# Optimization experiments

Measured on AMD Instinct MI355X. Metric: run time of the kernel, lower is better.

The kernel has to match this reference:

```python
import jax, jax.numpy as jnp
import numpy as np

POOL = 7          # cf.pool_size
SR = 2            # roi_align sampling_ratio
LEVELS = [0, 1, 2, 3]
C = 192           # cf.end_filts
HC = 2            # cf.head_classes
RF = 1
N_ROIS = 1000
B = 4


def roi_align_2d(fmap, boxes, batch_inds, pool_size=POOL, sr=SR):
    """Bilinear RoIAlign. fmap [B,C,H,W]; boxes [N,4] = (y1,x1,y2,x2) in fmap pixel coords."""
    _, _, H, W = fmap.shape
    y1, x1, y2, x2 = boxes[:, 0], boxes[:, 1], boxes[:, 2], boxes[:, 3]
    bin_h = jnp.maximum(y2 - y1, 1.0) / pool_size
    bin_w = jnp.maximum(x2 - x1, 1.0) / pool_size
    # sampling offsets within the roi, [pool*sr]
    grid = (jnp.arange(pool_size, dtype=jnp.float32)[:, None]
            + (jnp.arange(sr, dtype=jnp.float32)[None, :] + 0.5) / sr).reshape(-1)
    ys = y1[:, None] + grid[None, :] * bin_h[:, None]   # [N, P*S]
    xs = x1[:, None] + grid[None, :] * bin_w[:, None]   # [N, P*S]
    y = jnp.broadcast_to(ys[:, :, None], (ys.shape[0], ys.shape[1], xs.shape[1]))  # [N,PS,PS]
    x = jnp.broadcast_to(xs[:, None, :], y.shape)
    valid = (y >= -1.0) & (y <= H) & (x >= -1.0) & (x <= W)
    y = jnp.clip(y, 0.0, H - 1)
    x = jnp.clip(x, 0.0, W - 1)
    y0 = jnp.floor(y).astype(jnp.int32)
    x0 = jnp.floor(x).astype(jnp.int32)
    y1i = jnp.minimum(y0 + 1, H - 1)
    x1i = jnp.minimum(x0 + 1, W - 1)
    ly = y - y0
    lx = x - x0
    b = batch_inds[:, None, None]
    f00 = fmap[b, :, y0, x0]    # [N,PS,PS,C]
    f01 = fmap[b, :, y0, x1i]
    f10 = fmap[b, :, y1i, x0]
    f11 = fmap[b, :, y1i, x1i]
    w00 = ((1 - ly) * (1 - lx))[..., None]
    w01 = ((1 - ly) * lx)[..., None]
    w10 = (ly * (1 - lx))[..., None]
    w11 = (ly * lx)[..., None]
    val = (f00 * w00 + f01 * w01 + f10 * w10 + f11 * w11) * valid[..., None]
    n = val.shape[0]
    val = val.reshape(n, pool_size, sr, pool_size, sr, -1).mean(axis=(2, 4))  # [N,P,P,C]
    return jnp.transpose(val, (0, 3, 1, 2))  # [N,C,P,P]


def pyramid_roi_align(fmaps, rois, pool_size=POOL, levels=LEVELS):
    boxes = jax.lax.stop_gradient(rois[:, :4])  # level_boxes.detach() in original
    batch_ix = rois[:, 4].astype(jnp.int32)
    h = boxes[:, 2] - boxes[:, 0]
    w = boxes[:, 3] - boxes[:, 1]
    roi_level = jnp.clip(jnp.round(4.0 + jnp.log2(jnp.sqrt(h * w))),
                         levels[0], levels[-1]).astype(jnp.int32)
    pooled = jnp.zeros((boxes.shape[0], fmaps[0].shape[1], pool_size, pool_size), fmaps[0].dtype)
    for li, lvl in enumerate(levels):
        H, W = fmaps[li].shape[2], fmaps[li].shape[3]
        scale = jnp.asarray([H, W, H, W], jnp.float32)
        p = roi_align_2d(fmaps[li], boxes * scale, batch_ix, pool_size)
        pooled = jnp.where((roi_level == lvl)[:, None, None, None], p, pooled)
    return pooled


def setup_inputs() -> dict:
    key = jax.random.key(0)
    ks = jax.random.split(key, 20)
    fmap0 = jax.random.normal(ks[0], (B, C, 128, 128), jnp.float32)
    fmap1 = jax.random.normal(ks[1], (B, C, 64, 64), jnp.float32)
    fmap2 = jax.random.normal(ks[2], (B, C, 32, 32), jnp.float32)
    fmap3 = jax.random.normal(ks[3], (B, C, 16, 16), jnp.float32)
    # valid normalized rois: (y1,x1,y2,x2,batch_ix)
    cy = jax.random.uniform(ks[4], (N_ROIS,), minval=0.15, maxval=0.85)
    cx = jax.random.uniform(ks[5], (N_ROIS,), minval=0.15, maxval=0.85)
    hh = jax.random.uniform(ks[6], (N_ROIS,), minval=0.02, maxval=0.15)
    hw = jax.random.uniform(ks[7], (N_ROIS,), minval=0.02, maxval=0.15)
    bix = jax.random.randint(ks[8], (N_ROIS,), 0, B).astype(jnp.float32)
    rois = jnp.stack([jnp.clip(cy - hh, 0, 1), jnp.clip(cx - hw, 0, 1),
                      jnp.clip(cy + hh, 0, 1), jnp.clip(cx + hw, 0, 1), bix], axis=1)
    d = C * 4  # 768
    s1 = 1.0 / np.sqrt(C * POOL * POOL)
    s2 = 1.0 / np.sqrt(d)
    params = dict(
        w1=jax.random.normal(ks[9], (d, C, POOL, POOL), jnp.float32) * s1,
        b1=jnp.zeros((d,), jnp.float32),
        w2=jax.random.normal(ks[10], (d, d), jnp.float32) * s2,
        b2=jnp.zeros((d,), jnp.float32),
        w_bbox=jax.random.normal(ks[11], (HC * 4, d), jnp.float32) * s2,
        b_bbox=jnp.zeros((HC * 4,), jnp.float32),
        w_cls=jax.random.normal(ks[12], (HC, d), jnp.float32) * s2,
        b_cls=jnp.zeros((HC,), jnp.float32),
        w_reg=jax.random.normal(ks[13], (HC * RF, d), jnp.float32) * s2,
        b_reg=jnp.zeros((HC * RF,), jnp.float32),
        w_unc=jax.random.normal(ks[14], (HC, d), jnp.float32) * s2,
        b_unc=jnp.zeros((HC,), jnp.float32),
    )
    return dict(fmap0=fmap0, fmap1=fmap1, fmap2=fmap2, fmap3=fmap3, rois=rois, **params)


def reference(fmap0, fmap1, fmap2, fmap3, rois, w1, b1, w2, b2,
              w_bbox, b_bbox, w_cls, b_cls, w_reg, b_reg, w_unc, b_unc):
    x = pyramid_roi_align([fmap0, fmap1, fmap2, fmap3], rois)      # [N,C,7,7]
    x = jax.nn.relu(jnp.einsum('ncij,ocij->no', x, w1) + b1)       # conv1 ks=7 -> 1x1
    x = jax.nn.relu(x @ w2.T + b2)                                 # conv2 1x1
    n = x.shape[0]
    mrcnn_bbox = (x @ w_bbox.T + b_bbox).reshape(n, -1, 4)         # [N,HC,2*dim]
    mrcnn_class_logits = x @ w_cls.T + b_cls                       # [N,HC]
    reg = (x @ w_reg.T + b_reg).reshape(n, -1, RF)
    unc = x @ w_unc.T + b_unc
    mrcnn_regress = jnp.concatenate([reg, unc[..., None]], axis=2)  # [N,HC,RF+1]
    return mrcnn_bbox, mrcnn_class_logits, mrcnn_regress
```

## Files before the change

### kernel.cpp

```cpp
#include <hip/hip_runtime.h>
#include <hip/hip_bf16.h>
#include <cstddef>
#include <cstdint>

typedef __attribute__((ext_vector_type(8))) short short8;
typedef __attribute__((ext_vector_type(16))) float float16;

#define C_CH 192
#define PK   9408
#define D1   768

__device__ __forceinline__ ushort f2bf(float v) {
    return __builtin_bit_cast(unsigned short, __float2bfloat16(v));
}

__global__ __launch_bounds__(256) void cvt_bf16_2(
    const float* __restrict__ in1, ushort* __restrict__ out1, int n4_1,
    const float* __restrict__ in2, ushort* __restrict__ out2, int n4_2)
{
    int i = blockIdx.x * 256 + threadIdx.x;
    const float* in; ushort* out;
    if (i < n4_1) { in = in1; out = out1; }
    else          { i -= n4_1; if (i >= n4_2) return; in = in2; out = out2; }
    float4 v = ((const float4*)in)[i];
    ushort4 o;
    o.x = f2bf(v.x); o.y = f2bf(v.y); o.z = f2bf(v.z); o.w = f2bf(v.w);
    ((ushort4*)out)[i] = o;
}

__global__ __launch_bounds__(256) void cvt_bf16(const float* __restrict__ in,
                                                ushort* __restrict__ out, int n4)
{
    int i = blockIdx.x * 256 + threadIdx.x;
    if (i >= n4) return;
    float4 v = ((const float4*)in)[i];
    ushort4 o;
    o.x = f2bf(v.x); o.y = f2bf(v.y); o.z = f2bf(v.z); o.w = f2bf(v.w);
    ((ushort4*)out)[i] = o;
}

__global__ __launch_bounds__(256) void fused_pre(
    const float* __restrict__ f0, const float* __restrict__ f1,
    const float* __restrict__ f2, const float* __restrict__ f3,
    ushort* __restrict__ o0, ushort* __restrict__ o1,
    ushort* __restrict__ o2, ushort* __restrict__ o3,
    const float* __restrict__ w1src, ushort* __restrict__ w1dst, int n41,
    const float* __restrict__ w2src, ushort* __restrict__ w2dst, int n42,
    int nTrans)
{
    __shared__ unsigned int sm[96][33];

    int bx = blockIdx.x;
    if (bx >= nTrans) {
        int i = (bx - nTrans) * 256 + threadIdx.x;
        const float* in; ushort* out;
        if (i < n41) { in = w1src; out = w1dst; }
        else         { i -= n41; if (i >= n42) return; in = w2src; out = w2dst; }
        float4 v = ((const float4*)in)[i];
        ushort4 o;
        o.x = f2bf(v.x); o.y = f2bf(v.y); o.z = f2bf(v.z); o.w = f2bf(v.w);
        ((ushort4*)out)[i] = o;
        return;
    }

    int b = bx / 680;
    int t = bx - b * 680;
    const float* in; ushort* out; int HW, hw0;
    if      (t < 512) { in = f0; out = o0; HW = 16384; hw0 = t * 32; }
    else if (t < 640) { in = f1; out = o1; HW = 4096;  hw0 = (t - 512) * 32; }
    else if (t < 672) { in = f2; out = o2; HW = 1024;  hw0 = (t - 640) * 32; }
    else              { in = f3; out = o3; HW = 256;   hw0 = (t - 672) * 32; }

    int tx = threadIdx.x & 31;
    int ty = threadIdx.x >> 5;

    const float* ip = in + (size_t)b * C_CH * HW + hw0;
    #pragma unroll
    for (int it = 0; it < 12; ++it) {
        int cp = it * 8 + ty;
        float v0 = ip[(size_t)(2 * cp)     * HW + tx];
        float v1 = ip[(size_t)(2 * cp + 1) * HW + tx];
        sm[cp][tx] = (unsigned int)f2bf(v0) | ((unsigned int)f2bf(v1) << 16);
    }
    __syncthreads();

    unsigned int* op = (unsigned int*)(out + ((size_t)b * HW + hw0) * C_CH);
    #pragma unroll
    for (int it = 0; it < 12; ++it) {
        int idx = it * 256 + (int)threadIdx.x;
        int r = idx / 96;
        int p = idx - r * 96;
        op[idx] = sm[p][r];
    }
}

__global__ __launch_bounds__(192) void roi_gather(
    const ushort* __restrict__ n0p, const ushort* __restrict__ n1p,
    const ushort* __restrict__ n2p, const ushort* __restrict__ n3p,
    const float* __restrict__ rois, ushort* __restrict__ pooled)
{
    __shared__ float4 s_patch4[256 * 12];
    __shared__ int    s_off[196][4];
    __shared__ float  s_w[196][4];
    __shared__ ushort s_out[96 * 49];

    const int n    = blockIdx.x >> 1;
    const int half = blockIdx.x & 1;
    const int tid  = threadIdx.x;

    float by1 = rois[n*5+0], bx1 = rois[n*5+1];
    float by2 = rois[n*5+2], bx2 = rois[n*5+3];
    int   b   = (int)rois[n*5+4];

    float hh = by2 - by1, ww = bx2 - bx1;
    int lvl = (int)rintf(4.0f + log2f(sqrtf(hh * ww)));
    lvl = min(max(lvl, 0), 3);

    const ushort* fm; int H;
    if      (lvl == 0) { fm = n0p; H = 128; }
    else if (lvl == 1) { fm = n1p; H = 64;  }
    else if (lvl == 2) { fm = n2p; H = 32;  }
    else               { fm = n3p; H = 16;  }
    float Hf = (float)H;

    float y1p = by1 * Hf, x1p = bx1 * Hf;
    float y2p = by2 * Hf, x2p = bx2 * Hf;
    float bin_h = fmaxf(y2p - y1p, 1.0f) * (1.0f / 7.0f);
    float bin_w = fmaxf(x2p - x1p, 1.0f) * (1.0f / 7.0f);

    float yF = fminf(fmaxf(y1p + 0.25f * bin_h, 0.0f), Hf - 1.0f);
    float yL = fminf(fmaxf(y1p + 6.75f * bin_h, 0.0f), Hf - 1.0f);
    float xF = fminf(fmaxf(x1p + 0.25f * bin_w, 0.0f), Hf - 1.0f);
    float xL = fminf(fmaxf(x1p + 6.75f * bin_w, 0.0f), Hf - 1.0f);
    int ymin = (int)floorf(yF);
    int ymax = min((int)floorf(yL) + 1, H - 1);
    int xmin = (int)floorf(xF);
    int xmax = min((int)floorf(xL) + 1, H - 1);
    int nrows = ymax - ymin + 1;
    int ncols = xmax - xmin + 1;
    int np = nrows * ncols;
    bool usePatch = (np <= 256);

    uintptr_t bp = (uintptr_t)(fm + (size_t)b * H * H * C_CH);
    unsigned int blo = __builtin_amdgcn_readfirstlane((unsigned int)bp);
    unsigned int bhi = __builtin_amdgcn_readfirstlane((unsigned int)(bp >> 32));
    const char* sbase = (const char*)((((uintptr_t)bhi) << 32) | blo);

    for (int s = tid; s < 196; s += 192) {
        int sx = s & 1, sy = (s >> 1) & 1, ij = s >> 2;
        int i = ij / 7, j = ij - i * 7;

        float gy = (float)i + 0.25f + 0.5f * (float)sy;
        float y  = y1p + gy * bin_h;
        bool  vy = (y >= -1.0f) && (y <= Hf);
        float yc = fminf(fmaxf(y, 0.0f), Hf - 1.0f);
        int   y0 = (int)floorf(yc);
        float ly = yc - (float)y0;
        int   y1i = min(y0 + 1, H - 1);

        float gx = (float)j + 0.25f + 0.5f * (float)sx;
        float x  = x1p + gx * bin_w;
        bool  vx = (x >= -1.0f) && (x <= Hf);
        float xc = fminf(fmaxf(x, 0.0f), Hf - 1.0f);
        int   x0 = (int)floorf(xc);
        float lx = xc - (float)x0;
        int   x1i = min(x0 + 1, H - 1);

        float vm = (vy && vx) ? 0.25f : 0.0f;
        if (usePatch) {
            int ry0 = y0 - ymin, ry1 = y1i - ymin;
            int rx0 = x0 - xmin, rx1 = x1i - xmin;
            s_off[s][0] = (ry0 * ncols + rx0) * 48;
            s_off[s][1] = (ry0 * ncols + rx1) * 48;
            s_off[s][2] = (ry1 * ncols + rx0) * 48;
            s_off[s][3] = (ry1 * ncols + rx1) * 48;
        } else {
            s_off[s][0] = (y0  * H + x0 ) * (C_CH * 2);
            s_off[s][1] = (y0  * H + x1i) * (C_CH * 2);
            s_off[s][2] = (y1i * H + x0 ) * (C_CH * 2);
            s_off[s][3] = (y1i * H + x1i) * (C_CH * 2);
        }
        s_w[s][0] = (1.0f - ly) * (1.0f - lx) * vm;
        s_w[s][1] = (1.0f - ly) * lx * vm;
        s_w[s][2] = ly * (1.0f - lx) * vm;
        s_w[s][3] = ly * lx * vm;
    }

    if (usePatch) {
        int pq = tid / 12;
        int pd = tid - pq * 12;
        for (int p0 = 0; p0 < np; p0 += 16) {
            int p = p0 + pq;
            if (p < np) {
                int py = p / ncols;
                int px = p - py * ncols;
                const char* src = sbase +
                    ((size_t)((ymin + py) * H + (xmin + px)) * (C_CH * 2)
                     + half * 192 + pd * 16);
                s_patch4[p * 12 + pd] = *(const float4*)src;
            }
        }
    }
    __syncthreads();

    const int grp = tid / 48;
    const int ci  = tid - grp * 48;
    const int cl  = ci * 2;
    const int bin_lo = grp * 13;
    const int bin_hi = min(bin_lo + 13, 49);

    if (usePatch) {
        const unsigned int* patch_dw = (const unsigned int*)s_patch4;
        for (int bin = bin_lo; bin < bin_hi; ++bin) {
            float a0 = 0.0f, a1 = 0.0f;
            #pragma unroll
            for (int sub = 0; sub < 4; ++sub) {
                int s = bin * 4 + sub;
                #pragma unroll
                for (int tp = 0; tp < 4; ++tp) {
                    unsigned int u = patch_dw[s_off[s][tp] + ci];
                    float w = s_w[s][tp];
                    float lo = __builtin_bit_cast(float, u << 16);
                    float hi = __builtin_bit_cast(float, u & 0xffff0000u);
                    a0 = fmaf(lo, w, a0);
                    a1 = fmaf(hi, w, a1);
                }
            }
            s_out[(cl + 0) * 49 + bin] = f2bf(a0);
            s_out[(cl + 1) * 49 + bin] = f2bf(a1);
        }
    } else {
        const int c4g = half * 192 + ci * 4;
        for (int bin = bin_lo; bin < bin_hi; ++bin) {
            float a0 = 0.0f, a1 = 0.0f;
            #pragma unroll
            for (int sub = 0; sub < 4; ++sub) {
                int s = bin * 4 + sub;
                #pragma unroll
                for (int tp = 0; tp < 4; ++tp) {
                    unsigned int u = *(const unsigned int*)(sbase + (s_off[s][tp] + c4g));
                    float w = s_w[s][tp];
                    float lo = __builtin_bit_cast(float, u << 16);
                    float hi = __builtin_bit_cast(float, u & 0xffff0000u);
                    a0 = fmaf(lo, w, a0);
                    a1 = fmaf(hi, w, a1);
                }
            }
            s_out[(cl + 0) * 49 + bin] = f2bf(a0);
            s_out[(cl + 1) * 49 + bin] = f2bf(a1);
        }
    }
    __syncthreads();

    unsigned int* po = (unsigned int*)(pooled + (size_t)n * PK + half * 4704);
    const unsigned int* so = (const unsigned int*)s_out;
    for (int idx = tid; idx < 2352; idx += 192) po[idx] = so[idx];
}

__global__ __launch_bounds__(256) void roi_align_nchw(
    const float* __restrict__ f0, const float* __restrict__ f1,
    const float* __restrict__ f2, const float* __restrict__ f3,
    const float* __restrict__ rois, ushort* __restrict__ pooled, int n_rois)
{
    int idx = blockIdx.x * 256 + threadIdx.x;
    if (idx >= n_rois * PK) return;
    int n  = idx / PK;
    int r  = idx - n * PK;
    int c  = r / 49;
    int ij = r - c * 49;
    int i  = ij / 7;
    int j  = ij - i * 7;

    float by1 = rois[n*5+0], bx1 = rois[n*5+1];
    float by2 = rois[n*5+2], bx2 = rois[n*5+3];
    int   b   = (int)rois[n*5+4];

    float hh = by2 - by1, ww = bx2 - bx1;
    int lvl = (int)rintf(4.0f + log2f(sqrtf(hh * ww)));
    lvl = min(max(lvl, 0), 3);

    const float* fmap; int H;
    if      (lvl == 0) { fmap = f0; H = 128; }
    else if (lvl == 1) { fmap = f1; H = 64;  }
    else if (lvl == 2) { fmap = f2; H = 32;  }
    else               { fmap = f3; H = 16;  }
    float Hf = (float)H;

    float y1p = by1 * Hf, x1p = bx1 * Hf;
    float bin_h = fmaxf(by2 * Hf - y1p, 1.0f) * (1.0f / 7.0f);
    float bin_w = fmaxf(bx2 * Hf - x1p, 1.0f) * (1.0f / 7.0f);

    const float* base = fmap + ((size_t)b * C_CH + c) * (size_t)(H * H);

    float acc = 0.0f;
    #pragma unroll
    for (int sy = 0; sy < 2; ++sy) {
        float y  = y1p + ((float)i + 0.25f + 0.5f * (float)sy) * bin_h;
        bool  vy = (y >= -1.0f) && (y <= Hf);
        float yc = fminf(fmaxf(y, 0.0f), Hf - 1.0f);
        int   y0 = (int)floorf(yc);
        float ly = yc - (float)y0;
        int   y1i = min(y0 + 1, H - 1);
        #pragma unroll
        for (int sx = 0; sx < 2; ++sx) {
            float x  = x1p + ((float)j + 0.25f + 0.5f * (float)sx) * bin_w;
            bool  vx = (x >= -1.0f) && (x <= Hf);
            float xc = fminf(fmaxf(x, 0.0f), Hf - 1.0f);
            int   x0 = (int)floorf(xc);
            float lx = xc - (float)x0;
            int   x1i = min(x0 + 1, H - 1);
            if (vy && vx) {
                float v = base[y0 * H + x0 ] * (1.0f - ly) * (1.0f - lx)
                        + base[y0 * H + x1i] * (1.0f - ly) * lx
                        + base[y1i * H + x0 ] * ly * (1.0f - lx)
                        + base[y1i * H + x1i] * ly * lx;
                acc += v;
            }
        }
    }
    pooled[idx] = f2bf(acc * 0.25f);
}

template<int MODE>
__global__ __launch_bounds__(256) void mfma_gemm(
    const ushort* __restrict__ A, const ushort* __restrict__ W,
    const float* __restrict__ bias, void* __restrict__ outp,
    int M, int N, int K, int nkPer, int nkTotal)
{
    __shared__ char ldsA[2][8192];
    __shared__ char ldsB[2][8192];

    const int t    = threadIdx.x;
    const int lane = t & 63;
    const int wave = t >> 6;
    const int wm = wave >> 1, wn = wave & 1;

    const int m0 = blockIdx.y * 64;
    const int n0 = blockIdx.x * 64;
    const int kb = (MODE == 2) ? blockIdx.z * nkPer : 0;
    const int nk = (MODE == 2) ? min(nkPer, nkTotal - kb) : nkPer;

    const int ks   = t & 3;
    const int mrow = t >> 2;
    const int g    = mrow >> 5;
    const int rw   = mrow & 31;
    const int lof0 = ks*2048 + g*1024 + ((     rw) ^ (ks<<2))*16;
    const int lof1 = ks*2048 + g*1024 + ((32 + rw) ^ (ks<<2))*16;

    const int arow = min(m0 + mrow, M-1);
    const int brow = n0 + mrow;
    const ushort* ap = A + (size_t)arow * K + (size_t)kb * 64 + ks*16;
    const ushort* bp = W + (size_t)brow * K + (size_t)kb * 64 + ks*16;

    float4 ra0, ra1, rb0, rb1;
    float4 qa0, qa1, qb0, qb1;

    ra0 = ((const float4*)ap)[0]; ra1 = ((const float4*)ap)[1];
    rb0 = ((const float4*)bp)[0]; rb1 = ((const float4*)bp)[1];
    *(float4*)&ldsA[0][lof0] = ra0; *(float4*)&ldsA[0][lof1] = ra1;
    *(float4*)&ldsB[0][lof0] = rb0; *(float4*)&ldsB[0][lof1] = rb1;
    {
        int k1 = min(1, nk - 1);
        const ushort* ap1 = ap + (size_t)k1 * 64;
        const ushort* bp1 = bp + (size_t)k1 * 64;
        ra0 = ((const float4*)ap1)[0]; ra1 = ((const float4*)ap1)[1];
        rb0 = ((const float4*)bp1)[0]; rb1 = ((const float4*)bp1)[1];
    }
    __syncthreads();

    float16 acc = {};

    for (int kt = 0; kt < nk; ++kt) {
        {
            int k2 = min(kt + 2, nk - 1);
            const ushort* ap2 = ap + (size_t)k2 * 64;
            const ushort* bp2 = bp + (size_t)k2 * 64;
            qa0 = ((const float4*)ap2)[0]; qa1 = ((const float4*)ap2)[1];
            qb0 = ((const float4*)bp2)[0]; qb1 = ((const float4*)bp2)[1];
        }
        if (kt + 1 < nk) {
            char* dA = ldsA[(kt+1)&1]; char* dB = ldsB[(kt+1)&1];
            *(float4*)&dA[lof0] = ra0; *(float4*)&dA[lof1] = ra1;
            *(float4*)&dB[lof0] = rb0; *(float4*)&dB[lof1] = rb1;
        }
        const char* sA = ldsA[kt&1]; const char* sB = ldsB[kt&1];
        #pragma unroll
        for (int s = 0; s < 4; ++s) {
            int ro = s*2048 + (lane ^ (s<<2))*16;
            short8 af = *(const short8*)&sA[wm*1024 + ro];
            short8 bf = *(const short8*)&sB[wn*1024 + ro];
            acc = __builtin_amdgcn_mfma_f32_32x32x16_bf16(af, bf, acc, 0, 0, 0);
        }
        __syncthreads();
        ra0 = qa0; ra1 = qa1; rb0 = qb0; rb1 = qb1;
    }

    const int col   = lane & 31;
    const int rbase = 4 * (lane >> 5);
    const int nG    = n0 + wn*32 + col;

    if (MODE == 2) {
        float* O = (float*)outp + (size_t)blockIdx.z * M * N;
        #pragma unroll
        for (int r = 0; r < 16; ++r) {
            int row = (r & 3) + 8*(r >> 2) + rbase;
            int mG  = m0 + wm*32 + row;
            if (mG < M) O[(size_t)mG * N + nG] = acc[r];
        }
    } else if (MODE == 1) {
        const float bv = bias[nG];
        ushort* O = (ushort*)outp;
        #pragma unroll
        for (int r = 0; r < 16; ++r) {
            int row = (r & 3) + 8*(r >> 2) + rbase;
            int mG  = m0 + wm*32 + row;
            if (mG < M) O[(size_t)mG * N + nG] = f2bf(fmaxf(acc[r] + bv, 0.0f));
        }
    } else {
        const float bv = bias[nG];
        float* O = (float*)outp;
        #pragma unroll
        for (int r = 0; r < 16; ++r) {
            int row = (r & 3) + 8*(r >> 2) + rbase;
            int mG  = m0 + wm*32 + row;
            if (mG < M) O[(size_t)mG * N + nG] = fmaxf(acc[r] + bv, 0.0f);
        }
    }
}

__global__ __launch_bounds__(256) void mfma_gemm128(
    const ushort* __restrict__ A, const ushort* __restrict__ W,
    void* __restrict__ outp, int M, int N, int K, int nkPer, int nkTotal)
{
    __shared__ char ldsA[2][16384];
    __shared__ char ldsB[2][16384];

    const int t    = threadIdx.x;
    const int lane = t & 63;
    const int wave = t >> 6;
    const int wm = wave >> 1, wn = wave & 1;

    const int m0 = blockIdx.y * 128;
    const int n0 = blockIdx.x * 128;
    const int kb = blockIdx.z * nkPer;
    const int nk = min(nkPer, nkTotal - kb);

    const int ks   = t & 3;
    const int mrow = t >> 2;
    const int g    = mrow >> 5;
    const int rw   = mrow & 31;
    const int swz  = ks << 2;
    const int lof0 = ks*4096 + g*1024 + ((     rw) ^ swz)*16;
    const int lof1 = ks*4096 + g*1024 + ((32 + rw) ^ swz)*16;

    const int arow0 = min(m0 + mrow,      M-1);
    const int arow1 = min(m0 + mrow + 64, M-1);
    const int brow0 = n0 + mrow;
    const int brow1 = n0 + mrow + 64;
    const ushort* ap0 = A + (size_t)arow0 * K + (size_t)kb * 64 + ks*16;
    const ushort* ap1 = A + (size_t)arow1 * K + (size_t)kb * 64 + ks*16;
    const ushort* bp0 = W + (size_t)brow0 * K + (size_t)kb * 64 + ks*16;
    const ushort* bp1 = W + (size_t)brow1 * K + (size_t)kb * 64 + ks*16;

    float4 ra0, ra1, ra2, ra3, rb0, rb1, rb2, rb3;
    float4 qa0, qa1, qa2, qa3, qb0, qb1, qb2, qb3;

    ra0 = ((const float4*)ap0)[0]; ra1 = ((const float4*)ap0)[1];
    ra2 = ((const float4*)ap1)[0]; ra3 = ((const float4*)ap1)[1];
    rb0 = ((const float4*)bp0)[0]; rb1 = ((const float4*)bp0)[1];
    rb2 = ((const float4*)bp1)[0]; rb3 = ((const float4*)bp1)[1];
    *(float4*)&ldsA[0][lof0]      = ra0; *(float4*)&ldsA[0][lof1]      = ra1;
    *(float4*)&ldsA[0][lof0+2048] = ra2; *(float4*)&ldsA[0][lof1+2048] = ra3;
    *(float4*)&ldsB[0][lof0]      = rb0; *(float4*)&ldsB[0][lof1]      = rb1;
    *(float4*)&ldsB[0][lof0+2048] = rb2; *(float4*)&ldsB[0][lof1+2048] = rb3;
    {
        int k1 = min(1, nk - 1);
        const ushort* a0 = ap0 + (size_t)k1 * 64; const ushort* a1 = ap1 + (size_t)k1 * 64;
        const ushort* b0 = bp0 + (size_t)k1 * 64; const ushort* b1 = bp1 + (size_t)k1 * 64;
        ra0 = ((const float4*)a0)[0]; ra1 = ((const float4*)a0)[1];
        ra2 = ((const float4*)a1)[0]; ra3 = ((const float4*)a1)[1];
        rb0 = ((const float4*)b0)[0]; rb1 = ((const float4*)b0)[1];
        rb2 = ((const float4*)b1)[0]; rb3 = ((const float4*)b1)[1];
    }
    __syncthreads();

    float16 acc00 = {}, acc01 = {}, acc10 = {}, acc11 = {};

    for (int kt = 0; kt < nk; ++kt) {
        {
            int k2 = min(kt + 2, nk - 1);
            const ushort* a0 = ap0 + (size_t)k2 * 64; const ushort* a1 = ap1 + (size_t)k2 * 64;
            const ushort* b0 = bp0 + (size_t)k2 * 64; const ushort* b1 = bp1 + (size_t)k2 * 64;
            qa0 = ((const float4*)a0)[0]; qa1 = ((const float4*)a0)[1];
            qa2 = ((const float4*)a1)[0]; qa3 = ((const float4*)a1)[1];
            qb0 = ((const float4*)b0)[0]; qb1 = ((const float4*)b0)[1];
            qb2 = ((const float4*)b1)[0]; qb3 = ((const float4*)b1)[1];
        }
        if (kt + 1 < nk) {
            char* dA = ldsA[(kt+1)&1]; char* dB = ldsB[(kt+1)&1];
            *(float4*)&dA[lof0]      = ra0; *(float4*)&dA[lof1]      = ra1;
            *(float4*)&dA[lof0+2048] = ra2; *(float4*)&dA[lof1+2048] = ra3;
            *(float4*)&dB[lof0]      = rb0; *(float4*)&dB[lof1]      = rb1;
            *(float4*)&dB[lof0+2048] = rb2; *(float4*)&dB[lof1+2048] = rb3;
        }
        const char* sA = ldsA[kt&1]; const char* sB = ldsB[kt&1];
        #pragma unroll
        for (int s = 0; s < 4; ++s) {
            int ro = s*4096 + (lane ^ (s<<2))*16;
            short8 a0 = *(const short8*)&sA[wm*2048        + ro];
            short8 a1 = *(const short8*)&sA[wm*2048 + 1024 + ro];
            short8 b0 = *(const short8*)&sB[wn*2048        + ro];
            short8 b1 = *(const short8*)&sB[wn*2048 + 1024 + ro];
            acc00 = __builtin_amdgcn_mfma_f32_32x32x16_bf16(a0, b0, acc00, 0, 0, 0);
            acc01 = __builtin_amdgcn_mfma_f32_32x32x16_bf16(a0, b1, acc01, 0, 0, 0);
            acc10 = __builtin_amdgcn_mfma_f32_32x32x16_bf16(a1, b0, acc10, 0, 0, 0);
            acc11 = __builtin_amdgcn_mfma_f32_32x32x16_bf16(a1, b1, acc11, 0, 0, 0);
        }
        __syncthreads();
        ra0 = qa0; ra1 = qa1; ra2 = qa2; ra3 = qa3;
        rb0 = qb0; rb1 = qb1; rb2 = qb2; rb3 = qb3;
    }

    const int col   = lane & 31;
    const int rbase = 4 * (lane >> 5);
    float* O = (float*)outp + (size_t)blockIdx.z * M * N;

    const int mb0 = m0 + wm*64;
    const int nb0 = n0 + wn*64;
    #pragma unroll
    for (int r = 0; r < 16; ++r) {
        int row = (r & 3) + 8*(r >> 2) + rbase;
        int mG0 = mb0 + row;
        int mG1 = mb0 + 32 + row;
        int nG0 = nb0 + col;
        int nG1 = nb0 + 32 + col;
        if (mG0 < M) {
            O[(size_t)mG0 * N + nG0] = acc00[r];
            O[(size_t)mG0 * N + nG1] = acc01[r];
        }
        if (mG1 < M) {
            O[(size_t)mG1 * N + nG0] = acc10[r];
            O[(size_t)mG1 * N + nG1] = acc11[r];
        }
    }
}

__global__ __launch_bounds__(256) void reduce_relu_bf16(
    const float* __restrict__ P, const float* __restrict__ bias,
    ushort* __restrict__ Y, int MN, int N, int S)
{
    int idx = blockIdx.x * 256 + threadIdx.x;
    if (idx >= MN / 4) return;
    float4 s = ((const float4*)P)[idx];
    for (int k = 1; k < S; ++k) {
        float4 p = ((const float4*)(P + (size_t)k * MN))[idx];
        s.x += p.x; s.y += p.y; s.z += p.z; s.w += p.w;
    }
    int n4 = idx % (N / 4);
    float4 bv = ((const float4*)bias)[n4];
    ushort4 o;
    o.x = f2bf(fmaxf(s.x + bv.x, 0.0f));
    o.y = f2bf(fmaxf(s.y + bv.y, 0.0f));
    o.z = f2bf(fmaxf(s.z + bv.z, 0.0f));
    o.w = f2bf(fmaxf(s.w + bv.w, 0.0f));
    ((ushort4*)Y)[idx] = o;
}

__global__ __launch_bounds__(256) void reduce_heads(
    const float* __restrict__ P2, const float* __restrict__ b2, int S, int MN,
    const float* __restrict__ w_bbox, const float* __restrict__ b_bbox,
    const float* __restrict__ w_cls,  const float* __restrict__ b_cls,
    const float* __restrict__ w_reg,  const float* __restrict__ b_reg,
    const float* __restrict__ w_unc,  const float* __restrict__ b_unc,
    float* __restrict__ out, int n_rois)
{
    __shared__ float zrow[D1];
    const int m   = blockIdx.x;
    const int tid = threadIdx.x;

    const float* Pm = P2 + (size_t)m * D1;
    #pragma unroll
    for (int r = 0; r < 3; ++r) {
        int k = r * 256 + tid;
        float v = Pm[k];
        for (int s = 1; s < S; ++s) v += Pm[(size_t)s * MN + k];
        zrow[k] = fmaxf(v + b2[k], 0.0f);
    }
    __syncthreads();

    const int wave = tid >> 6;
    const int lane = tid & 63;
    for (int o = wave; o < 14; o += 4) {
        const float* w; float bb;
        if      (o < 8)  { w = w_bbox + o * D1;        bb = b_bbox[o]; }
        else if (o < 10) { w = w_cls  + (o - 8) * D1;  bb = b_cls[o - 8]; }
        else if (o < 12) { w = w_reg  + (o - 10) * D1; bb = b_reg[o - 10]; }
        else             { w = w_unc  + (o - 12) * D1; bb = b_unc[o - 12]; }
        float p = 0.0f;
        #pragma unroll
        for (int r = 0; r < 12; ++r) {
            int k = r * 64 + lane;
            p = fmaf(zrow[k], w[k], p);
        }
        #pragma unroll
        for (int d = 32; d >= 1; d >>= 1) p += __shfl_down(p, d, 64);
        if (lane == 0) {
            int off;
            int clsOff = n_rois * 8;
            int regOff = n_rois * 10;
            if      (o < 8)  off = m * 8 + o;
            else if (o < 10) off = clsOff + m * 2 + (o - 8);
            else if (o < 12) off = regOff + m * 4 + (o - 10) * 2;
            else             off = regOff + m * 4 + (o - 12) * 2 + 1;
            out[off] = p + bb;
        }
    }
}

__global__ __launch_bounds__(256) void heads_kernel(
    const float* __restrict__ Z,
    const float* __restrict__ w_bbox, const float* __restrict__ b_bbox,
    const float* __restrict__ w_cls,  const float* __restrict__ b_cls,
    const float* __restrict__ w_reg,  const float* __restrict__ b_reg,
    const float* __restrict__ w_unc,  const float* __restrict__ b_unc,
    float* __restrict__ out, int n_rois)
{
    int idx = blockIdx.x * 256 + threadIdx.x;
    if (idx >= n_rois * 14) return;
    int n = idx / 14;
    int o = idx - n * 14;

    const float* w; float bb;
    if      (o < 8)  { w = w_bbox + o * D1;        bb = b_bbox[o]; }
    else if (o < 10) { w = w_cls  + (o - 8) * D1;  bb = b_cls[o - 8]; }
    else if (o < 12) { w = w_reg  + (o - 10) * D1; bb = b_reg[o - 10]; }
    else             { w = w_unc  + (o - 12) * D1; bb = b_unc[o - 12]; }

    const float* z = Z + (size_t)n * D1;
    float s = bb;
    for (int k = 0; k < D1; k += 4) {
        float4 zv = *(const float4*)(z + k);
        float4 wv = *(const float4*)(w + k);
        s = fmaf(zv.x, wv.x, s);
        s = fmaf(zv.y, wv.y, s);
        s = fmaf(zv.z, wv.z, s);
        s = fmaf(zv.w, wv.w, s);
    }

    int off;
    int clsOff = n_rois * 8;
    int regOff = n_rois * 10;
    if      (o < 8)  off = n * 8 + o;
    else if (o < 10) off = clsOff + n * 2 + (o - 8);
    else if (o < 12) off = regOff + n * 4 + (o - 10) * 2;
    else             off = regOff + n * 4 + (o - 12) * 2 + 1;
    out[off] = s;
}

extern "C" void kernel_launch(void* const* d_in, const int* in_sizes, int n_in,
                              void* d_out, int out_size, void* d_ws, size_t ws_size,
                              hipStream_t stream)
{
    const float* f0   = (const float*)d_in[0];
    const float* f1   = (const float*)d_in[1];
    const float* f2   = (const float*)d_in[2];
    const float* f3   = (const float*)d_in[3];
    const float* rois = (const float*)d_in[4];
    const float* w1   = (const float*)d_in[5];
    const float* b1   = (const float*)d_in[6];
    const float* w2   = (const float*)d_in[7];
    const float* b2   = (const float*)d_in[8];
    const float* w_bbox = (const float*)d_in[9];
    const float* b_bbox = (const float*)d_in[10];
    const float* w_cls  = (const float*)d_in[11];
    const float* b_cls  = (const float*)d_in[12];
    const float* w_reg  = (const float*)d_in[13];
    const float* b_reg  = (const float*)d_in[14];
    const float* w_unc  = (const float*)d_in[15];
    const float* b_unc  = (const float*)d_in[16];
    float* out = (float*)d_out;

    const int n_rois = in_sizes[4] / 5;
    const int B      = in_sizes[0] / (C_CH * 128 * 128);

    const size_t nh0B = (size_t)B * 16384 * C_CH * 2;
    const size_t nh1B = (size_t)B * 4096  * C_CH * 2;
    const size_t nh2B = (size_t)B * 1024  * C_CH * 2;
    const size_t nh3B = (size_t)B * 256   * C_CH * 2;
    const size_t nhAll = nh0B + nh1B + nh2B + nh3B;
    const size_t poolB = (size_t)n_rois * PK * 2;
    const size_t w1Bb  = (size_t)D1 * PK * 2;
    const size_t w2Bb  = (size_t)D1 * D1 * 2;
    const size_t Yb    = (size_t)n_rois * D1 * 2;
    const size_t Zb    = (size_t)n_rois * D1 * 4;
    const size_t smallB = w2Bb + Yb + Zb;

    const int SPLIT1  = 10;
    const int SPLIT1F = 5;
    const int SPLIT2  = 2;

    const size_t P1b   = (size_t)SPLIT1 * n_rois * D1 * 4;
    const size_t needX2 = nhAll + poolB + w1Bb + w2Bb + Yb;
    const size_t needX  = nhAll + poolB + smallB;

    char* ws = (char*)d_ws;

    int n41 = D1*PK/4, n42 = D1*D1/4;

    if (ws_size >= needX2) {
        ushort* nh0 = (ushort*)ws;
        ushort* nh1 = nh0 + nh0B/2;
        ushort* nh2 = nh1 + nh1B/2;
        ushort* nh3 = nh2 + nh2B/2;
        ushort* pooledB = (ushort*)(ws + nhAll);
        ushort* w1B = (ushort*)(ws + nhAll + poolB);
        ushort* w2B = (ushort*)(ws + nhAll + poolB + w1Bb);
        ushort* Y   = (ushort*)(ws + nhAll + poolB + w1Bb + w2Bb);
        float*  P   = (float*)ws;
        float*  P2  = (float*)(ws + P1b);

        int nTrans = 680 * B;
        int nCvt   = (n41 + n42 + 255) / 256;
        fused_pre<<<nTrans + nCvt, 256, 0, stream>>>(
            f0, f1, f2, f3, nh0, nh1, nh2, nh3,
            w1, w1B, n41, w2, w2B, n42, nTrans);

        roi_gather<<<2 * n_rois, 192, 0, stream>>>(nh0, nh1, nh2, nh3, rois, pooledB);

        {
            int nkTotal = PK / 64;
            int nkPer   = (nkTotal + SPLIT1 - 1) / SPLIT1;
            dim3 grid(D1/128, (n_rois + 127)/128, SPLIT1);
            mfma_gemm128<<<grid, 256, 0, stream>>>(pooledB, w1B, P,
                                                   n_rois, D1, PK, nkPer, nkTotal);
            int MN = n_rois * D1;
            reduce_relu_bf16<<<(MN/4 + 255)/256, 256, 0, stream>>>(P, b1, Y, MN, D1, SPLIT1);
        }
        {
            int nkTotal = D1 / 64;
            int nkPer   = nkTotal / SPLIT2;
            dim3 grid(D1/64, (n_rois + 63)/64, SPLIT2);
            mfma_gemm<2><<<grid, 256, 0, stream>>>(Y, w2B, nullptr, P2,
                                                   n_rois, D1, D1, nkPer, nkTotal);
            int MN = n_rois * D1;
            reduce_heads<<<n_rois, 256, 0, stream>>>(P2, b2, SPLIT2, MN,
                w_bbox, b_bbox, w_cls, b_cls, w_reg, b_reg, w_unc, b_unc, out, n_rois);
        }
    } else if (ws_size >= needX) {
        ushort* nh0 = (ushort*)ws;
        ushort* nh1 = nh0 + nh0B/2;
        ushort* nh2 = nh1 + nh1B/2;
        ushort* nh3 = nh2 + nh2B/2;
        ushort* w1B = (ushort*)ws;
        float*  P   = (float*)(ws + w1Bb);
        float*  P2  = (float*)ws;
        ushort* pooledB = (ushort*)(ws + nhAll);
        ushort* w2B = (ushort*)(ws + nhAll + poolB);
        ushort* Y   = w2B + w2Bb/2;

        int nTrans = 680 * B;
        fused_pre<<<nTrans, 256, 0, stream>>>(
            f0, f1, f2, f3, nh0, nh1, nh2, nh3,
            w1, (ushort*)nullptr, 0, w2, (ushort*)nullptr, 0, nTrans);
        roi_gather<<<2 * n_rois, 192, 0, stream>>>(nh0, nh1, nh2, nh3, rois, pooledB);
        cvt_bf16_2<<<(n41 + n42 + 255)/256, 256, 0, stream>>>(
            w1, w1B, n41, w2, w2B, n42);
        {
            int nkTotal = PK / 64;
            int nkPer   = (nkTotal + SPLIT1F - 1) / SPLIT1F;
            dim3 grid(D1/64, (n_rois + 63)/64, SPLIT1F);
            mfma_gemm<2><<<grid, 256, 0, stream>>>(pooledB, w1B, nullptr, P,
                                                   n_rois, D1, PK, nkPer, nkTotal);
            int MN = n_rois * D1;
            reduce_relu_bf16<<<(MN/4 + 255)/256, 256, 0, stream>>>(P, b1, Y, MN, D1, SPLIT1F);
        }
        {
            int nkTotal = D1 / 64;
            int nkPer   = nkTotal / SPLIT2;
            dim3 grid(D1/64, (n_rois + 63)/64, SPLIT2);
            mfma_gemm<2><<<grid, 256, 0, stream>>>(Y, w2B, nullptr, P2,
                                                   n_rois, D1, D1, nkPer, nkTotal);
            int MN = n_rois * D1;
            reduce_heads<<<n_rois, 256, 0, stream>>>(P2, b2, SPLIT2, MN,
                w_bbox, b_bbox, w_cls, b_cls, w_reg, b_reg, w_unc, b_unc, out, n_rois);
        }
    } else {
        ushort* pooledB = (ushort*)ws;
        ushort* w1B = pooledB + poolB/2;
        ushort* w2B = w1B + w1Bb/2;
        ushort* Y   = w2B + w2Bb/2;
        float*  Z   = (float*)((char*)Y + Yb);

        cvt_bf16<<<((D1*PK/4) + 255)/256, 256, 0, stream>>>(w1, w1B, D1*PK/4);
        cvt_bf16<<<((D1*D1/4) + 255)/256, 256, 0, stream>>>(w2, w2B, D1*D1/4);
        {
            int total = n_rois * PK;
            roi_align_nchw<<<(total + 255)/256, 256, 0, stream>>>(
                f0, f1, f2, f3, rois, pooledB, n_rois);
        }
        {
            dim3 grid(D1/64, (n_rois + 63)/64);
            mfma_gemm<1><<<grid, 256, 0, stream>>>(pooledB, w1B, b1, Y,
                                                   n_rois, D1, PK, PK/64, PK/64);
        }
        {
            dim3 grid(D1/64, (n_rois + 63)/64);
            mfma_gemm<0><<<grid, 256, 0, stream>>>(Y, w2B, b2, Z,
                                                   n_rois, D1, D1, D1/64, D1/64);
        }
        heads_kernel<<<(n_rois*14 + 255)/256, 256, 0, stream>>>(
            Z, w_bbox, b_bbox, w_cls, b_cls, w_reg, b_reg, w_unc, b_unc, out, n_rois);
    }
}
```

Baseline: 241.5 us.

## Replace LDS patch staging in roi_gather with double-buffered direct global gathers

Drops the shared-memory patch path and always gathers the four bilinear corner samples straight from global (L2-cached) memory. Each thread now handles 4 channels with 8-byte loads, and the loads for the next bin are issued into a register double buffer before the current bin is accumulated, to hide gather latency. Removing the 48KB patch buffer and setting launch bounds (192,4) aims at higher occupancy. The cost is more global/L2 traffic for overlapping samples and higher register pressure from the 32 float2 buffers.

```diff
diff --git a/kernel.cpp b/kernel.cpp
--- a/kernel.cpp
+++ b/kernel.cpp
@@ -94,13 +94,39 @@
     }
 }
 
-__global__ __launch_bounds__(192) void roi_gather(
+__device__ __forceinline__ void issue16w(
+    const char* sbase, const int (*offB)[4], int s4, int c8, float2* u)
+{
+    #pragma unroll
+    for (int k = 0; k < 16; ++k) {
+        int s  = s4 + (k >> 2);
+        int tp = k & 3;
+        u[k] = *(const float2*)(sbase + (offB[s][tp] + c8));
+    }
+}
+
+__device__ __forceinline__ void comp16w(
+    const float2* u, const float (*wt)[4], int s4,
+    float& a0, float& a1, float& a2, float& a3)
+{
+    #pragma unroll
+    for (int k = 0; k < 16; ++k) {
+        float w = wt[s4 + (k >> 2)][k & 3];
+        unsigned int u0 = __builtin_bit_cast(unsigned int, u[k].x);
+        unsigned int u1 = __builtin_bit_cast(unsigned int, u[k].y);
+        a0 = fmaf(__builtin_bit_cast(float, u0 << 16),         w, a0);
+        a1 = fmaf(__builtin_bit_cast(float, u0 & 0xffff0000u), w, a1);
+        a2 = fmaf(__builtin_bit_cast(float, u1 << 16),         w, a2);
+        a3 = fmaf(__builtin_bit_cast(float, u1 & 0xffff0000u), w, a3);
+    }
+}
+
+__global__ __launch_bounds__(192, 4) void roi_gather(
     const ushort* __restrict__ n0p, const ushort* __restrict__ n1p,
     const ushort* __restrict__ n2p, const ushort* __restrict__ n3p,
     const float* __restrict__ rois, ushort* __restrict__ pooled)
 {
-    __shared__ float4 s_patch4[256 * 12];
-    __shared__ int    s_off[196][4];
+    __shared__ int    s_offB[196][4];
     __shared__ float  s_w[196][4];
     __shared__ ushort s_out[96 * 49];
 
@@ -127,19 +153,6 @@
     float y2p = by2 * Hf, x2p = bx2 * Hf;
     float bin_h = fmaxf(y2p - y1p, 1.0f) * (1.0f / 7.0f);
     float bin_w = fmaxf(x2p - x1p, 1.0f) * (1.0f / 7.0f);
-
-    float yF = fminf(fmaxf(y1p + 0.25f * bin_h, 0.0f), Hf - 1.0f);
-    float yL = fminf(fmaxf(y1p + 6.75f * bin_h, 0.0f), Hf - 1.0f);
-    float xF = fminf(fmaxf(x1p + 0.25f * bin_w, 0.0f), Hf - 1.0f);
-    float xL = fminf(fmaxf(x1p + 6.75f * bin_w, 0.0f), Hf - 1.0f);
-    int ymin = (int)floorf(yF);
-    int ymax = min((int)floorf(yL) + 1, H - 1);
-    int xmin = (int)floorf(xF);
-    int xmax = min((int)floorf(xL) + 1, H - 1);
-    int nrows = ymax - ymin + 1;
-    int ncols = xmax - xmin + 1;
-    int np = nrows * ncols;
-    bool usePatch = (np <= 256);
 
     uintptr_t bp = (uintptr_t)(fm + (size_t)b * H * H * C_CH);
     unsigned int blo = __builtin_amdgcn_readfirstlane((unsigned int)bp);
@@ -167,88 +180,49 @@
         int   x1i = min(x0 + 1, H - 1);
 
         float vm = (vy && vx) ? 0.25f : 0.0f;
-        if (usePatch) {
-            int ry0 = y0 - ymin, ry1 = y1i - ymin;
-            int rx0 = x0 - xmin, rx1 = x1i - xmin;
-            s_off[s][0] = (ry0 * ncols + rx0) * 48;
-            s_off[s][1] = (ry0 * ncols + rx1) * 48;
-            s_off[s][2] = (ry1 * ncols + rx0) * 48;
-            s_off[s][3] = (ry1 * ncols + rx1) * 48;
-        } else {
-            s_off[s][0] = (y0  * H + x0 ) * (C_CH * 2);
-            s_off[s][1] = (y0  * H + x1i) * (C_CH * 2);
-            s_off[s][2] = (y1i * H + x0 ) * (C_CH * 2);
-            s_off[s][3] = (y1i * H + x1i) * (C_CH * 2);
-        }
+        s_offB[s][0] = (y0  * H + x0 ) * (C_CH * 2);
+        s_offB[s][1] = (y0  * H + x1i) * (C_CH * 2);
+        s_offB[s][2] = (y1i * H + x0 ) * (C_CH * 2);
+        s_offB[s][3] = (y1i * H + x1i) * (C_CH * 2);
         s_w[s][0] = (1.0f - ly) * (1.0f - lx) * vm;
         s_w[s][1] = (1.0f - ly) * lx * vm;
         s_w[s][2] = ly * (1.0f - lx) * vm;
         s_w[s][3] = ly * lx * vm;
     }
-
-    if (usePatch) {
-        int pq = tid / 12;
-        int pd = tid - pq * 12;
-        for (int p0 = 0; p0 < np; p0 += 16) {
-            int p = p0 + pq;
-            if (p < np) {
-                int py = p / ncols;
-                int px = p - py * ncols;
-                const char* src = sbase +
-                    ((size_t)((ymin + py) * H + (xmin + px)) * (C_CH * 2)
-                     + half * 192 + pd * 16);
-                s_patch4[p * 12 + pd] = *(const float4*)src;
-            }
-        }
-    }
     __syncthreads();
 
-    const int grp = tid / 48;
-    const int ci  = tid - grp * 48;
-    const int cl  = ci * 2;
-    const int bin_lo = grp * 13;
-    const int bin_hi = min(bin_lo + 13, 49);
-
-    if (usePatch) {
-        const unsigned int* patch_dw = (const unsigned int*)s_patch4;
-        for (int bin = bin_lo; bin < bin_hi; ++bin) {
-            float a0 = 0.0f, a1 = 0.0f;
-            #pragma unroll
-            for (int sub = 0; sub < 4; ++sub) {
-                int s = bin * 4 + sub;
-                #pragma unroll
-                for (int tp = 0; tp < 4; ++tp) {
-                    unsigned int u = patch_dw[s_off[s][tp] + ci];
-                    float w = s_w[s][tp];
-                    float lo = __builtin_bit_cast(float, u << 16);
-                    float hi = __builtin_bit_cast(float, u & 0xffff0000u);
-                    a0 = fmaf(lo, w, a0);
-                    a1 = fmaf(hi, w, a1);
-                }
-            }
+    const int grp = tid / 24;
+    const int ci  = tid - grp * 24;
+    const int cl  = ci * 4;
+    const int c8  = half * 192 + ci * 8;
+    const int bin_lo = (grp * 49) >> 3;
+    const int bin_hi = ((grp + 1) * 49) >> 3;
+
+    float2 ua[16], ub[16];
+
+    issue16w(sbase, s_offB, bin_lo * 4, c8, ua);
+    int bin = bin_lo;
+    while (true) {
+        if (bin + 1 < bin_hi) issue16w(sbase, s_offB, (bin + 1) * 4, c8, ub);
+        {
+            float a0 = 0.0f, a1 = 0.0f, a2 = 0.0f, a3 = 0.0f;
+            comp16w(ua, s_w, bin * 4, a0, a1, a2, a3);
             s_out[(cl + 0) * 49 + bin] = f2bf(a0);
             s_out[(cl + 1) * 49 + bin] = f2bf(a1);
-        }
-    } else {
-        const int c4g = half * 192 + ci * 4;
-        for (int bin = bin_lo; bin < bin_hi; ++bin) {
-            float a0 = 0.0f, a1 = 0.0f;
-            #pragma unroll
-            for (int sub = 0; sub < 4; ++sub) {
-                int s = bin * 4 + sub;
-                #pragma unroll
-                for (int tp = 0; tp < 4; ++tp) {
-                    unsigned int u = *(const unsigned int*)(sbase + (s_off[s][tp] + c4g));
-                    float w = s_w[s][tp];
-                    float lo = __builtin_bit_cast(float, u << 16);
-                    float hi = __builtin_bit_cast(float, u & 0xffff0000u);
-                    a0 = fmaf(lo, w, a0);
-                    a1 = fmaf(hi, w, a1);
-                }
-            }
+            s_out[(cl + 2) * 49 + bin] = f2bf(a2);
+            s_out[(cl + 3) * 49 + bin] = f2bf(a3);
+        }
+        if (++bin >= bin_hi) break;
+        if (bin + 1 < bin_hi) issue16w(sbase, s_offB, (bin + 1) * 4, c8, ua);
+        {
+            float a0 = 0.0f, a1 = 0.0f, a2 = 0.0f, a3 = 0.0f;
+            comp16w(ub, s_w, bin * 4, a0, a1, a2, a3);
             s_out[(cl + 0) * 49 + bin] = f2bf(a0);
             s_out[(cl + 1) * 49 + bin] = f2bf(a1);
-        }
+            s_out[(cl + 2) * 49 + bin] = f2bf(a2);
+            s_out[(cl + 3) * 49 + bin] = f2bf(a3);
+        }
+        if (++bin >= bin_hi) break;
     }
     __syncthreads();
 
```

Measured after the change: 228.9 us. 1.05x faster.
